# Optimization experiments

Hardware: AMD Instinct MI355X
Metric: run time of the kernel (lower is better)

## Reference

```python
import jax, jax.numpy as jnp
import numpy as np
from jax import lax

ANCHOR_AREAS = (128.0**2, 256.0**2, 512.0**2)
ASPECT_RATIOS = (0.5, 1.0, 2.0)
STRIDE = 32.0                      # resnet backbone: get_orig_stat maps fm -> input via x*32
PRE_NMS_TOP_N = 2000
POST_NMS_TOP_N = 100
NMS_IOU_T = 0.7
SCORE_T = 0.1
MIN_SCALE = 0.01
BBOX_XFORM_CLIP = float(np.log(1000.0 / 16.0))


def make_anchors(H, W):
    # anchors laid out in (H, W, A) order to match the offset permutation below
    sizes = []
    for area in ANCHOR_AREAS:
        for r in ASPECT_RATIOS:          # aspect_ratio = w / h
            sizes.append((np.sqrt(area * r), np.sqrt(area / r)))
    sizes = jnp.asarray(np.asarray(sizes, dtype=np.float32))  # [A, 2] (w, h)
    cy = (jnp.arange(H, dtype=jnp.float32) + 0.5) * STRIDE
    cx = (jnp.arange(W, dtype=jnp.float32) + 0.5) * STRIDE
    cyg, cxg = jnp.meshgrid(cy, cx, indexing='ij')             # [H, W]
    cxg = cxg[:, :, None]
    cyg = cyg[:, :, None]
    w = sizes[:, 0]
    h = sizes[:, 1]
    anchors = jnp.stack([cxg - w / 2, cyg - h / 2, cxg + w / 2, cyg + h / 2], axis=-1)
    return anchors.reshape(-1, 4)                              # [H*W*A, 4] xyxy


def decode_boxes(anchors, offsets):
    # anchors [N,4], offsets [B,N,4] (tx, ty, tw, th) -> boxes [B,N,4] xyxy
    wa = anchors[:, 2] - anchors[:, 0]
    ha = anchors[:, 3] - anchors[:, 1]
    cxa = anchors[:, 0] + 0.5 * wa
    cya = anchors[:, 1] + 0.5 * ha
    tx, ty = offsets[..., 0], offsets[..., 1]
    tw = jnp.minimum(offsets[..., 2], BBOX_XFORM_CLIP)
    th = jnp.minimum(offsets[..., 3], BBOX_XFORM_CLIP)
    px = tx * wa + cxa
    py = ty * ha + cya
    pw = jnp.exp(tw) * wa
    ph = jnp.exp(th) * ha
    return jnp.stack([px - pw / 2, py - ph / 2, px + pw / 2, py + ph / 2], axis=-1)


def box_iou(a, b):
    area_a = (a[:, 2] - a[:, 0]) * (a[:, 3] - a[:, 1])
    area_b = (b[:, 2] - b[:, 0]) * (b[:, 3] - b[:, 1])
    lt = jnp.maximum(a[:, None, :2], b[None, :, :2])
    rb = jnp.minimum(a[:, None, 2:], b[None, :, 2:])
    wh = jnp.clip(rb - lt, 0.0)
    inter = wh[..., 0] * wh[..., 1]
    return inter / (area_a[:, None] + area_b[None, :] - inter + 1e-9)


def nms_single(boxes, scores):
    # boxes [P,4] sorted by descending score; invalid entries carry score -1
    P = boxes.shape[0]
    iou = box_iou(boxes, boxes)
    idx = jnp.arange(P)

    def body(i, keep):
        sup = (iou[i] > NMS_IOU_T) & (idx > i)
        return jnp.where(keep[i], keep & (~sup), keep)

    keep = lax.stop_gradient(lax.fori_loop(0, P, body, scores > 0.0))
    kept_scores = jnp.where(keep, scores, -1.0)
    top_s, top_i = lax.top_k(kept_scores, POST_NMS_TOP_N)
    return boxes[top_i], top_s


def rpn_forward(features, W1, b1, W2, b2, W3, b3):
    B, Cin, H, W = features.shape
    A = W3.shape[0]
    # 3x3 sliding conv + ReLU
    t = lax.conv_general_dilated(
        features, W1, window_strides=(1, 1), padding='SAME',
        dimension_numbers=('NCHW', 'OIHW', 'NCHW'))
    t = jax.nn.relu(t + b1[None, :, None, None])
    # 1x1 sibling heads as channel contractions
    offs = jnp.einsum('bchw,oc->bohw', t, W2) + b2[None, :, None, None]   # [B, A*4, H, W]
    logits = jnp.einsum('bchw,oc->bohw', t, W3) + b3[None, :, None, None]  # [B, A, H, W]
    # reorder to per-anchor layout (H, W, A)
    offs = offs.reshape(B, A, 4, H, W).transpose(0, 3, 4, 1, 2).reshape(B, -1, 4)
    scores = jax.nn.sigmoid(logits.transpose(0, 2, 3, 1).reshape(B, -1))  # [B, N]
    anchors = make_anchors(H, W)
    boxes = decode_boxes(anchors, offs)                                    # [B, N, 4]
    # clip to image boundary (handle_cross_boundary_boxes during testing)
    img_w, img_h = W * STRIDE, H * STRIDE
    boxes = jnp.stack([
        jnp.clip(boxes[..., 0], 0.0, img_w),
        jnp.clip(boxes[..., 1], 0.0, img_h),
        jnp.clip(boxes[..., 2], 0.0, img_w),
        jnp.clip(boxes[..., 3], 0.0, img_h)], axis=-1)
    # score-threshold + min-scale filtering
    bw = boxes[..., 2] - boxes[..., 0]
    bh = boxes[..., 3] - boxes[..., 1]
    valid = (scores >= SCORE_T) & (bw > MIN_SCALE * img_w) & (bh > MIN_SCALE * img_h)
    masked = jnp.where(valid, scores, -1.0)
    # pre-NMS top-k, then per-image NMS + post-NMS top-n
    top_s, top_i = lax.top_k(masked, PRE_NMS_TOP_N)                        # [B, P]
    top_boxes = jnp.take_along_axis(boxes, top_i[..., None], axis=1)       # [B, P, 4]
    out_boxes, out_scores = jax.vmap(nms_single)(top_boxes, top_s)
    return out_boxes, out_scores                                           # [B,100,4], [B,100]


def setup_inputs() -> dict:
    key = jax.random.key(0)
    ks = jax.random.split(key, 4)
    B, Cin, H, W = 8, 1024, 50, 50
    A = 9
    C = 512
    return {
        'features': jax.random.normal(ks[0], (B, Cin, H, W), jnp.float32),
        'W1': jax.random.normal(ks[1], (C, Cin, 3, 3), jnp.float32) * 0.01,
        'b1': jnp.zeros((C,), jnp.float32),
        'W2': jax.random.normal(ks[2], (A * 4, C), jnp.float32) * 0.01,
        'b2': jnp.zeros((A * 4,), jnp.float32),
        'W3': jax.random.normal(ks[3], (A, C), jnp.float32) * 0.01,
        'b3': jnp.zeros((A,), jnp.float32),
    }


def reference(features, W1, b1, W2, b2, W3, b3):
    return rpn_forward(features, W1, b1, W2, b2, W3, b3)
```

## Files before the change

kernel.cpp:

```cpp
#include <hip/hip_runtime.h>
#include <cstdint>

#define NB 8
#define CIN 1024
#define HDIM 50
#define WDIM 50
#define COUT 512
#define NA 9
#define NANCH (HDIM*WDIM*NA)
#define PRE_N 2000
#define POST_N 100

typedef __attribute__((ext_vector_type(8))) short bf16x8;
typedef __attribute__((ext_vector_type(4))) float f32x4;
typedef __attribute__((ext_vector_type(16))) float f32x16;
typedef __attribute__((ext_vector_type(8))) unsigned short ushort8v;

constexpr size_t TPLANE    = 20578304;
constexpr size_t OFF_TPH   = 0;
constexpr size_t OFF_TPL   = 20578304;
constexpr size_t OFF_BOXES = 41156608;
constexpr size_t OFF_KEYS  = 44036608;
constexpr size_t OFF_TBOX  = 45476608;
constexpr size_t OFF_TS    = 45732608;
constexpr size_t OFF_SUP   = 45796608;
constexpr size_t QDIM      = 2976;
constexpr size_t PLSTRIDE  = QDIM * 8;
constexpr size_t PPLANE    = 48758784;
constexpr size_t OFF_PH    = 49892864;
constexpr size_t OFF_PL    = OFF_PH + PPLANE;
constexpr size_t WPLANE    = 9437184;
constexpr size_t OFF_WH    = 147410432;
constexpr size_t OFF_WL    = OFF_WH + WPLANE;

__device__ __forceinline__ void split2bf16(float v, unsigned short &hi, unsigned short &lo) {
    unsigned int u = __float_as_uint(v);
    unsigned int r = u + 0x7FFFu + ((u >> 16) & 1u);
    hi = (unsigned short)(r >> 16);
    float hf = __uint_as_float(((unsigned int)hi) << 16);
    float lf = v - hf;
    unsigned int u2 = __float_as_uint(lf);
    unsigned int r2 = u2 + 0x7FFFu + ((u2 >> 16) & 1u);
    lo = (unsigned short)(r2 >> 16);
}

__device__ __forceinline__ void gl_lds(const unsigned short* g, unsigned short* l) {
    __builtin_amdgcn_global_load_lds(
        (const __attribute__((address_space(1))) unsigned int*)(const void*)g,
        (__attribute__((address_space(3))) unsigned int*)(void*)l,
        16, 0, 0);
}

struct StageOn  { static constexpr bool value = true;  };
struct StageOff { static constexpr bool value = false; };

__global__ __launch_bounds__(256) void prep_all(const float* __restrict__ f,
                                                const float* __restrict__ W1,
                                                unsigned short* __restrict__ Ph,
                                                unsigned short* __restrict__ Pl,
                                                unsigned short* __restrict__ Wh,
                                                unsigned short* __restrict__ Wl) {
    int blk = blockIdx.x;
    if (blk < 5952) {
        int id = blk * 256 + threadIdx.x;
        int q = id % (int)QDIM; int r = id / (int)QDIM;
        int cic = r % 64; int b = r / 64;
        int pp = q - 53;
        int rr = pp / 52, cc = pp - rr * 52;
        int h = rr - 1, w = cc - 1;
        bool inb = (pp >= 0) && (pp < 2704) && (h >= 0) && (h < HDIM) && (w >= 0) && (w < WDIM);
        ushort8v hv0, lv0, hv1, lv1;
#pragma unroll
        for (int j = 0; j < 16; ++j) {
            float v = 0.f;
            if (inb) v = f[(((size_t)b * CIN + cic * 16 + j) * HDIM + h) * WDIM + w];
            unsigned short hi, lo;
            split2bf16(v, hi, lo);
            if (j < 8) { hv0[j] = hi; lv0[j] = lo; }
            else       { hv1[j - 8] = hi; lv1[j - 8] = lo; }
        }
        size_t b0 = ((size_t)((b * 64 + cic) * 2 + 0)) * PLSTRIDE + (size_t)q * 8;
        size_t b1 = ((size_t)((b * 64 + cic) * 2 + 1)) * PLSTRIDE + (size_t)q * 8;
        *(ushort8v*)&Ph[b0] = hv0;
        *(ushort8v*)&Ph[b1] = hv1;
        *(ushort8v*)&Pl[b0] = lv0;
        *(ushort8v*)&Pl[b1] = lv1;
    } else {
        int id = (blk - 5952) * 256 + threadIdx.x;
        int co = id % 64; int r = id / 64;
        int cic = r % 64; int cot = r / 64;
        int cog = cot * 64 + co;
        const float* src = W1 + ((size_t)cog * CIN + cic * 16) * 9;
        float v[144];
#pragma unroll
        for (int i = 0; i < 36; ++i) {
            float4 x = ((const float4*)src)[i];
            v[i * 4 + 0] = x.x; v[i * 4 + 1] = x.y; v[i * 4 + 2] = x.z; v[i * 4 + 3] = x.w;
        }
#pragma unroll
        for (int tap = 0; tap < 9; ++tap) {
            ushort8v hv0, lv0, hv1, lv1;
#pragma unroll
            for (int j = 0; j < 16; ++j) {
                unsigned short hi, lo;
                split2bf16(v[j * 9 + tap], hi, lo);
                if (j < 8) { hv0[j] = hi; lv0[j] = lo; }
                else       { hv1[j - 8] = hi; lv1[j - 8] = lo; }
            }
            size_t base = (((size_t)(cot * 64 + cic) * 9 + tap) * 2) * 512;
            *(ushort8v*)&Wh[base + co * 8]       = hv0;
            *(ushort8v*)&Wh[base + 512 + co * 8] = hv1;
            *(ushort8v*)&Wl[base + co * 8]       = lv0;
            *(ushort8v*)&Wl[base + 512 + co * 8] = lv1;
        }
    }
}


#define MFMA12(A_, B_)                                                               \
    do {                                                                             \
        _Pragma("unroll") for (int s_ = 0; s_ < 3; ++s_)                             \
        _Pragma("unroll") for (int jm_ = 0; jm_ < 2; ++jm_)                          \
        _Pragma("unroll") for (int jn_ = 0; jn_ < 2; ++jn_) {                        \
            const bf16x8 &av_ = (s_ == 2) ? A_[jm_][1] : A_[jm_][0];                 \
            const bf16x8 &bv_ = (s_ == 1) ? B_[jn_][1] : B_[jn_][0];                 \
            acc[jm_][jn_] = __builtin_amdgcn_mfma_f32_32x32x16_bf16(                 \
                av_, bv_, acc[jm_][jn_], 0, 0, 0);                                   \
        }                                                                            \
    } while (0)

#define LOADF(A_, B_, TL_)                                                           \
    do {                                                                             \
        const int dlt_ = (tg - 1) * 52 + ((TL_) - 1);                                \
        _Pragma("unroll") for (int jm_ = 0; jm_ < 2; ++jm_) {                        \
            int ad_ = ((wv * 2 + jm_) * 32 + lm + dlt_ + 53) * 8;                    \
            A_[jm_][0] = *(const bf16x8*)&bA[(0 * 2 + lk) * 3072 + ad_];             \
            A_[jm_][1] = *(const bf16x8*)&bA[(1 * 2 + lk) * 3072 + ad_];             \
        }                                                                            \
        _Pragma("unroll") for (int jn_ = 0; jn_ < 2; ++jn_) {                        \
            int bd_ = (TL_) * 1024 + lk * 512 + (jn_ * 32 + lm) * 8;                 \
            B_[jn_][0] = *(const bf16x8*)&bB[bd_];                                   \
            B_[jn_][1] = *(const bf16x8*)&bB[3072 + bd_];                            \
        }                                                                            \
    } while (0)

__global__ __launch_bounds__(256, 2) void conv_mfma(const unsigned short* __restrict__ FPh,
                                                    const unsigned short* __restrict__ FPl,
                                                    const unsigned short* __restrict__ WPh,
                                                    const unsigned short* __restrict__ WPl,
                                                    const float* __restrict__ b1,
                                                    unsigned short* __restrict__ Tph,
                                                    unsigned short* __restrict__ Tpl) {
    extern __shared__ unsigned short smem[];
    unsigned short* const Abase = smem;
    unsigned short* const Bbase = smem + 24576;

    int blk = blockIdx.x;
    int logical = (blk & 7) * 88 + (blk >> 3);
    int cot = logical & 7;
    int ptile = (logical >> 3) % 11;
    int b = logical / 88;
    int co0 = cot * 64;
    int P0 = 32 + ptile * 256;

    int t = threadIdx.x, wv = t >> 6, ln = t & 63;
    int lm = ln & 31, lk = ln >> 5;

    f32x16 acc[2][2];
#pragma unroll
    for (int jm = 0; jm < 2; ++jm)
#pragma unroll
        for (int jn = 0; jn < 2; ++jn)
#pragma unroll
            for (int rg = 0; rg < 16; ++rg) acc[jm][jn][rg] = 0.f;

    auto stageA = [&](int buf, int cic, int ac) {
        int hl = ac / 12, lkc = (ac / 6) & 1, s = ac % 6;
        const unsigned short* pl = hl ? FPl : FPh;
        const unsigned short* src = pl
            + ((size_t)((b * 64 + cic) * 2 + lkc)) * PLSTRIDE
            + (size_t)P0 * 8 + s * 512 + ln * 8;
        gl_lds(src, &Abase[buf * 12288 + (hl * 2 + lkc) * 3072 + s * 512]);
    };
    auto stageB = [&](int buf, int cic, int tg, int c) {
        int hl = c / 6, j = c % 6;
        const unsigned short* pl = hl ? WPl : WPh;
        const unsigned short* src = pl + (size_t)(cot * 64 + cic) * 9216
            + (size_t)(tg * 6 + j) * 512 + ln * 8;
        gl_lds(src, &Bbase[buf * 6144 + hl * 3072 + j * 512]);
    };

#pragma unroll
    for (int k = 0; k < 9; ++k) {
        int id = wv * 9 + k;
        if (id < 24) stageA(0, 0, id);
        else         stageB(0, 0, 0, id - 24);
    }
    __syncthreads();

    auto do_cic = [&](int cic, auto stage_c) {
        constexpr bool STAGE = decltype(stage_c)::value;
        int abuf = cic & 1;
#pragma unroll
        for (int tg = 0; tg < 3; ++tg) {
            int bbuf = (cic + tg) & 1;
            if (STAGE || tg < 2) {
                int cicb = (tg == 2) ? cic + 1 : cic;
                int tgn  = (tg == 2) ? 0 : tg + 1;
#pragma unroll
                for (int j = 0; j < 3; ++j) stageB(bbuf ^ 1, cicb, tgn, wv * 3 + j);
            }
            if constexpr (STAGE) {
#pragma unroll
                for (int j = 0; j < 2; ++j) stageA(abuf ^ 1, cic + 1, tg * 8 + wv * 2 + j);
            }
            const unsigned short* bA = Abase + abuf * 12288;
            const unsigned short* bB = Bbase + bbuf * 6144;

            bf16x8 aX[2][2], bX[2][2], aY[2][2], bY[2][2];
            LOADF(aX, bX, 0);
            __builtin_amdgcn_s_setprio(1);
            LOADF(aY, bY, 1);
            MFMA12(aX, bX);
            LOADF(aX, bX, 2);
            MFMA12(aY, bY);
            MFMA12(aX, bX);
            __builtin_amdgcn_s_setprio(0);

            if constexpr (STAGE) {
                __builtin_amdgcn_sched_group_barrier(0x070, 5, 0);
                __builtin_amdgcn_sched_group_barrier(0x100, 8, 0);
#pragma unroll
                for (int g = 0; g < 8; ++g) {
                    __builtin_amdgcn_sched_group_barrier(0x008, 3, 0);
                    __builtin_amdgcn_sched_group_barrier(0x100, 2, 0);
                }
                __builtin_amdgcn_sched_group_barrier(0x008, 12, 0);
            }
            __syncthreads();
        }
    };

#pragma unroll 1
    for (int cic = 0; cic < 63; ++cic) do_cic(cic, StageOn{});
    do_cic(63, StageOff{});

#pragma unroll
    for (int jn = 0; jn < 2; ++jn) {
        int co = co0 + jn * 32 + lm;
        float bv = b1[co];
#pragma unroll
        for (int jm = 0; jm < 2; ++jm) {
#pragma unroll
            for (int rg = 0; rg < 16; ++rg) {
                int mrow = (rg & 3) + 8 * (rg >> 2) + 4 * lk;
                int pp = P0 + (wv * 2 + jm) * 32 + mrow;
                int rr = pp / 52, cc = pp - rr * 52;
                int h = rr - 1, w = cc - 1;
                if ((unsigned)h < HDIM && (unsigned)w < WDIM) {
                    float v = fmaxf(acc[jm][jn][rg] + bv, 0.f);
                    unsigned short hi, lo;
                    split2bf16(v, hi, lo);
                    int px = b * 2500 + h * 50 + w;
                    size_t sa = (((((size_t)(px >> 7) * 16 + (co >> 5)) * 8 + ((px >> 4) & 7)) * 4
                                  + ((co >> 3) & 3)) * 16 + (px & 15)) * 8 + (co & 7);
                    Tph[sa] = hi;
                    Tpl[sa] = lo;
                }
            }
        }
    }
}

__global__ __launch_bounds__(256) void proj_decode_mfma(const unsigned short* __restrict__ Tph,
                                                        const unsigned short* __restrict__ Tpl,
                                                        const float* __restrict__ W2,
                                                        const float* __restrict__ b2,
                                                        const float* __restrict__ W3,
                                                        const float* __restrict__ b3,
                                                        float* __restrict__ boxes,
                                                        unsigned long long* __restrict__ keys) {
    __shared__ unsigned short sTh[4096], sTl[4096];
    __shared__ unsigned short sWh[1536], sWl[1536];
    __shared__ float pout[128 * 46];

    int blk = blockIdx.x;
    int px0 = blk * 128;
    int t = threadIdx.x, wv = t >> 6, ln = t & 63;
    int lm = ln & 15, q = ln >> 4;

    f32x4 acc[2][3];
#pragma unroll
    for (int jm = 0; jm < 2; ++jm)
#pragma unroll
        for (int nf = 0; nf < 3; ++nf) acc[jm][nf] = (f32x4){0.f, 0.f, 0.f, 0.f};

#pragma unroll 1
    for (int cc16 = 0; cc16 < 16; ++cc16) {
        __syncthreads();
        size_t base = ((size_t)blk * 16 + cc16) * 4096;
        if (wv == 0) {
#pragma unroll
            for (int s = 0; s < 4; ++s) gl_lds(Tph + base + s * 512 + ln * 8, &sTh[s * 512]);
        } else if (wv == 1) {
#pragma unroll
            for (int s = 4; s < 8; ++s) gl_lds(Tph + base + s * 512 + ln * 8, &sTh[s * 512]);
        } else if (wv == 2) {
#pragma unroll
            for (int s = 0; s < 4; ++s) gl_lds(Tpl + base + s * 512 + ln * 8, &sTl[s * 512]);
        } else {
#pragma unroll
            for (int s = 4; s < 8; ++s) gl_lds(Tpl + base + s * 512 + ln * 8, &sTl[s * 512]);
        }
        int c0 = cc16 * 32;
        for (int idx = t; idx < 1536; idx += 256) {
            int o = idx >> 5, ci = idx & 31;
            float v = 0.f;
            if (o < 36) v = W2[o * 512 + c0 + ci];
            else if (o < 45) v = W3[(o - 36) * 512 + c0 + ci];
            unsigned short hi, lo;
            split2bf16(v, hi, lo);
            int ad = (((o >> 4) * 4 + (ci >> 3)) * 16 + (o & 15)) * 8 + (ci & 7);
            sWh[ad] = hi; sWl[ad] = lo;
        }
        __syncthreads();

        bf16x8 a[2][2], bb[3][2];
#pragma unroll
        for (int jm = 0; jm < 2; ++jm) {
            int mf = wv * 2 + jm;
            int ad = ((mf * 4 + q) * 16 + lm) * 8;
            a[jm][0] = *(const bf16x8*)&sTh[ad];
            a[jm][1] = *(const bf16x8*)&sTl[ad];
        }
#pragma unroll
        for (int nf = 0; nf < 3; ++nf) {
            int ad = ((nf * 4 + q) * 16 + lm) * 8;
            bb[nf][0] = *(const bf16x8*)&sWh[ad];
            bb[nf][1] = *(const bf16x8*)&sWl[ad];
        }
#pragma unroll
        for (int jm = 0; jm < 2; ++jm)
#pragma unroll
            for (int nf = 0; nf < 3; ++nf) {
                acc[jm][nf] = __builtin_amdgcn_mfma_f32_16x16x32_bf16(a[jm][0], bb[nf][0], acc[jm][nf], 0, 0, 0);
                acc[jm][nf] = __builtin_amdgcn_mfma_f32_16x16x32_bf16(a[jm][0], bb[nf][1], acc[jm][nf], 0, 0, 0);
                acc[jm][nf] = __builtin_amdgcn_mfma_f32_16x16x32_bf16(a[jm][1], bb[nf][0], acc[jm][nf], 0, 0, 0);
            }
    }
    __syncthreads();
#pragma unroll
    for (int jm = 0; jm < 2; ++jm)
#pragma unroll
        for (int nf = 0; nf < 3; ++nf) {
            int o = nf * 16 + lm;
            if (o < 45) {
                float bias = (o < 36) ? b2[o] : b3[o - 36];
#pragma unroll
                for (int rg = 0; rg < 4; ++rg) {
                    int pxl = (wv * 2 + jm) * 16 + q * 4 + rg;
                    pout[pxl * 46 + o] = acc[jm][nf][rg] + bias;
                }
            }
        }
    __syncthreads();

    const float AW[9] = {90.50966799187809f, 128.0f, 181.01933598375618f,
                         181.01933598375618f, 256.0f, 362.03867196751236f,
                         362.03867196751236f, 512.0f, 724.0773439350247f};
    const float AH[9] = {181.01933598375618f, 128.0f, 90.50966799187809f,
                         362.03867196751236f, 256.0f, 181.01933598375618f,
                         724.0773439350247f, 512.0f, 362.03867196751236f};
    const float CLIPV = 4.135166556742356f;
    const float IMG = 1600.0f;

    for (int it = t; it < 128 * 9; it += 256) {
        int pxl = it / 9, a = it - pxl * 9;
        int pxg = px0 + pxl;
        if (pxg >= 20000) continue;
        int b = pxg / 2500, rem = pxg % 2500;
        int h = rem / 50, w = rem % 50;

        float tx = pout[pxl * 46 + a * 4 + 0];
        float ty = pout[pxl * 46 + a * 4 + 1];
        float tw = pout[pxl * 46 + a * 4 + 2];
        float th = pout[pxl * 46 + a * 4 + 3];
        float lg = pout[pxl * 46 + 36 + a];

        float s = 1.0f / (1.0f + expf(-lg));

        float cx = ((float)w + 0.5f) * 32.0f;
        float cy = ((float)h + 0.5f) * 32.0f;
        float x1a = cx - 0.5f * AW[a];
        float x2a = cx + 0.5f * AW[a];
        float y1a = cy - 0.5f * AH[a];
        float y2a = cy + 0.5f * AH[a];
        float waf = x2a - x1a;
        float haf = y2a - y1a;
        float cxa = x1a + 0.5f * waf;
        float cya = y1a + 0.5f * haf;

        float twc = tw < CLIPV ? tw : CLIPV;
        float thc = th < CLIPV ? th : CLIPV;
        float pxc = tx * waf + cxa;
        float pyc = ty * haf + cya;
        float pw  = expf(twc) * waf;
        float ph  = expf(thc) * haf;

        float x1 = pxc - 0.5f * pw;
        float y1 = pyc - 0.5f * ph;
        float x2 = pxc + 0.5f * pw;
        float y2 = pyc + 0.5f * ph;
        x1 = fminf(fmaxf(x1, 0.f), IMG);
        y1 = fminf(fmaxf(y1, 0.f), IMG);
        x2 = fminf(fmaxf(x2, 0.f), IMG);
        y2 = fminf(fmaxf(y2, 0.f), IMG);

        float bw = x2 - x1, bh = y2 - y1;
        bool valid = (s >= 0.1f) && (bw > 16.0f) && (bh > 16.0f);
        float m = valid ? s : -1.0f;

        int idx = (h * WDIM + w) * NA + a;
        size_t gi = (size_t)b * NANCH + idx;
        ((float4*)boxes)[gi] = make_float4(x1, y1, x2, y2);
        unsigned int u = __float_as_uint(m);
        unsigned int k32 = (u & 0x80000000u) ? ~u : (u | 0x80000000u);
        keys[gi] = ((unsigned long long)k32 << 15) | (unsigned long long)(32767 - idx);
    }
}

__global__ __launch_bounds__(1024) void select_sort_kernel(const unsigned long long* __restrict__ keys,
                                                           const float* __restrict__ boxes,
                                                           float* __restrict__ top_boxes,
                                                           float* __restrict__ top_s) {
    int b = blockIdx.x;
    int t = threadIdx.x;
    int wv = t >> 6;
    const unsigned long long* kb = keys + (size_t)b * NANCH;

    __shared__ unsigned int whist[16][256];
    __shared__ unsigned int hist[256];
    __shared__ int s_chosen, s_rnew, s_done;
    __shared__ unsigned int s_cnt;
    __shared__ unsigned long long skeys[2048];

    const int widths[6] = {8, 8, 8, 8, 8, 7};
    unsigned long long prefix = 0;
    int bitsdone = 0;
    int r = PRE_N;

    if (t == 0) s_done = 0;

    for (int p = 0; p < 6; ++p) {
        int width = widths[p];
        int bins = 1 << width;
        int shift = 47 - bitsdone - width;
        for (int i = t; i < 16 * 256; i += 1024) ((unsigned int*)whist)[i] = 0;
        __syncthreads();
        for (int i = t; i < NANCH; i += 1024) {
            unsigned long long k = kb[i];
            if ((k >> (47 - bitsdone)) == prefix)
                atomicAdd(&whist[wv][(unsigned)((k >> shift) & (unsigned long long)(bins - 1))], 1u);
        }
        __syncthreads();
        if (t < bins) {
            unsigned int s = 0;
#pragma unroll
            for (int w = 0; w < 16; ++w) s += whist[w][t];
            hist[t] = s;
        }
        __syncthreads();
        if (t == 0) {
            int acc = 0, chosen = 0, rnew = 1;
            for (int d = bins - 1; d >= 0; --d) {
                int hv = (int)hist[d];
                if (acc + hv >= r) {
                    chosen = d; rnew = r - acc;
                    if ((PRE_N - r) + acc + hv <= 2048) s_done = 1;
                    break;
                }
                acc += hv;
            }
            s_chosen = chosen;
            s_rnew = rnew;
        }
        __syncthreads();
        prefix = (prefix << width) | (unsigned long long)s_chosen;
        bitsdone += width;
        r = s_rnew;
        __syncthreads();
        if (s_done) break;
    }
    unsigned long long Kst = prefix << (47 - bitsdone);

    if (t == 0) s_cnt = 0;
    __syncthreads();
    for (int i = t; i < NANCH; i += 1024) {
        unsigned long long k = kb[i];
        if (k >= Kst) {
            unsigned int p = atomicAdd(&s_cnt, 1u);
            if (p < 2048) skeys[p] = k;
        }
    }
    __syncthreads();
    unsigned int cnt = s_cnt;
    for (int i = t; i < 2048; i += 1024)
        if (i >= (int)cnt) skeys[i] = 0ull;
    for (int k = 2; k <= 2048; k <<= 1) {
        for (int j = k >> 1; j > 0; j >>= 1) {
            __syncthreads();
            for (int i = t; i < 2048; i += 1024) {
                int l = i ^ j;
                if (l > i) {
                    unsigned long long a = skeys[i], c = skeys[l];
                    bool up = ((i & k) == 0);
                    if (up ? (a < c) : (a > c)) { skeys[i] = c; skeys[l] = a; }
                }
            }
        }
    }
    __syncthreads();
    for (int i = t; i < PRE_N; i += 1024) {
        unsigned long long k = skeys[i];
        unsigned int k32 = (unsigned int)(k >> 15);
        float m = (k32 & 0x80000000u) ? __uint_as_float(k32 & 0x7FFFFFFFu)
                                      : __uint_as_float(~k32);
        unsigned int idx = 32767u - (unsigned int)(k & 32767ull);
        size_t gi = (size_t)b * NANCH + idx;
        top_s[b * PRE_N + i] = m;
        ((float4*)top_boxes)[b * PRE_N + i] = ((const float4*)boxes)[gi];
    }
}

__global__ __launch_bounds__(256) void sup_kernel(const float* __restrict__ top_boxes,
                                                  unsigned long long* __restrict__ supm) {
    int blk = blockIdx.x;
    int b = blk / 125;
    int chunk = blk % 125;
    int t = threadIdx.x;

    __shared__ float bx1[PRE_N], by1[PRE_N], bx2[PRE_N], by2[PRE_N];
    for (int i = t; i < PRE_N; i += 256) {
        float4 v = ((const float4*)top_boxes)[b * PRE_N + i];
        bx1[i] = v.x; by1[i] = v.y; bx2[i] = v.z; by2[i] = v.w;
    }
    __syncthreads();

    int wave = t >> 6, lane = t & 63;
    for (int rr = 0; rr < 4; ++rr) {
        int i = chunk * 16 + wave * 4 + rr;
        float ax1 = bx1[i], ay1 = by1[i], ax2 = bx2[i], ay2 = by2[i];
        float aarea = (ax2 - ax1) * (ay2 - ay1);
        for (int jw = 0; jw < 32; ++jw) {
            int j = jw * 64 + lane;
            bool sup = false;
            if (j > i && j < PRE_N) {
                float jx1 = bx1[j], jy1 = by1[j], jx2 = bx2[j], jy2 = by2[j];
                float ix1 = fmaxf(ax1, jx1), iy1 = fmaxf(ay1, jy1);
                float ix2 = fminf(ax2, jx2), iy2 = fminf(ay2, jy2);
                float iw = fmaxf(ix2 - ix1, 0.f);
                float ih = fmaxf(iy2 - iy1, 0.f);
                float inter = iw * ih;
                float barea = (jx2 - jx1) * (jy2 - jy1);
                float iou = inter / (aarea + barea - inter + 1e-9f);
                sup = iou > 0.7f;
            }
            unsigned long long m = __ballot(sup);
            if (lane == 0) supm[((size_t)b * PRE_N + i) * 32 + jw] = m;
        }
    }
}

__global__ __launch_bounds__(256) void nms_fin_kernel(const float* __restrict__ top_s,
                                                      const unsigned long long* __restrict__ supm,
                                                      const float* __restrict__ top_boxes,
                                                      float* __restrict__ out) {
    int b = blockIdx.x;
    int t = threadIdx.x;
    __shared__ unsigned int kw[64];
    __shared__ int wpre[65];

    if (t < 64) {
        int lane = t;
        unsigned int alive = 0;
        for (int q = 0; q < 32; ++q) {
            int i = lane * 32 + q;
            if (i < PRE_N && top_s[b * PRE_N + i] > 0.f) alive |= (1u << q);
        }
        const unsigned long long* sm = supm + (size_t)b * PRE_N * 32;
        const unsigned int* sup32 = (const unsigned int*)sm;

        for (int tt = 0; tt < 32; ++tt) {
            unsigned int alo = __shfl(alive, 2 * tt);
            unsigned int ahi = __shfl(alive, 2 * tt + 1);
            unsigned long long talive = (unsigned long long)alo | ((unsigned long long)ahi << 32);
            int i_row = tt * 64 + lane;
            unsigned long long rm = (i_row < PRE_N) ? sm[(size_t)i_row * 32 + tt] : 0ull;

            unsigned long long kept = 0, rem = talive;
            while (rem) {
                int j = __builtin_ctzll(rem);
                kept |= (1ull << j);
                unsigned long long rmj = __shfl(rm, j);
                rem &= ~rmj;
                rem &= ~(1ull << j);
            }

            unsigned int oracc = 0;
            unsigned long long kk = kept;
            while (kk) {
                int j0 = __builtin_ctzll(kk); kk &= kk - 1;
                int j1 = -1, j2 = -1, j3 = -1, j4 = -1, j5 = -1, j6 = -1, j7 = -1;
                if (kk) { j1 = __builtin_ctzll(kk); kk &= kk - 1; }
                if (kk) { j2 = __builtin_ctzll(kk); kk &= kk - 1; }
                if (kk) { j3 = __builtin_ctzll(kk); kk &= kk - 1; }
                if (kk) { j4 = __builtin_ctzll(kk); kk &= kk - 1; }
                if (kk) { j5 = __builtin_ctzll(kk); kk &= kk - 1; }
                if (kk) { j6 = __builtin_ctzll(kk); kk &= kk - 1; }
                if (kk) { j7 = __builtin_ctzll(kk); kk &= kk - 1; }
                unsigned int v0 = sup32[(size_t)(tt * 64 + j0) * 64 + lane];
                unsigned int v1 = (j1 >= 0) ? sup32[(size_t)(tt * 64 + j1) * 64 + lane] : 0u;
                unsigned int v2 = (j2 >= 0) ? sup32[(size_t)(tt * 64 + j2) * 64 + lane] : 0u;
                unsigned int v3 = (j3 >= 0) ? sup32[(size_t)(tt * 64 + j3) * 64 + lane] : 0u;
                unsigned int v4 = (j4 >= 0) ? sup32[(size_t)(tt * 64 + j4) * 64 + lane] : 0u;
                unsigned int v5 = (j5 >= 0) ? sup32[(size_t)(tt * 64 + j5) * 64 + lane] : 0u;
                unsigned int v6 = (j6 >= 0) ? sup32[(size_t)(tt * 64 + j6) * 64 + lane] : 0u;
                unsigned int v7 = (j7 >= 0) ? sup32[(size_t)(tt * 64 + j7) * 64 + lane] : 0u;
                oracc |= (v0 | v1) | (v2 | v3) | (v4 | v5) | (v6 | v7);
            }
            alive &= ~oracc;
            if (lane == 2 * tt)     alive = (unsigned int)kept;
            if (lane == 2 * tt + 1) alive = (unsigned int)(kept >> 32);
        }
        kw[lane] = alive;
    }
    __syncthreads();
    if (t == 0) {
        int run = 0;
        for (int w = 0; w < 64; ++w) { wpre[w] = run; run += __popc(kw[w]); }
        wpre[64] = run;
    }
    __syncthreads();
    int total = wpre[64];
    float* out_boxes  = out;
    float* out_scores = out + NB * POST_N * 4;
    for (int i = t; i < PRE_N; i += 256) {
        unsigned int w = kw[i >> 5];
        bool kept = (w >> (i & 31)) & 1u;
        int rk = wpre[i >> 5] + __popc(w & ((1u << (i & 31)) - 1u));
        int pos = kept ? rk : total + (i - rk);
        if (pos < POST_N) {
            out_scores[b * POST_N + pos] = kept ? top_s[b * PRE_N + i] : -1.0f;
            ((float4*)out_boxes)[b * POST_N + pos] = ((const float4*)top_boxes)[b * PRE_N + i];
        }
    }
}

extern "C" void kernel_launch(void* const* d_in, const int* in_sizes, int n_in,
                              void* d_out, int out_size, void* d_ws, size_t ws_size,
                              hipStream_t stream) {
    const float* features = (const float*)d_in[0];
    const float* W1 = (const float*)d_in[1];
    const float* b1 = (const float*)d_in[2];
    const float* W2 = (const float*)d_in[3];
    const float* b2 = (const float*)d_in[4];
    const float* W3 = (const float*)d_in[5];
    const float* b3 = (const float*)d_in[6];
    float* out = (float*)d_out;
    char* ws = (char*)d_ws;

    unsigned short* Tph = (unsigned short*)(ws + OFF_TPH);
    unsigned short* Tpl = (unsigned short*)(ws + OFF_TPL);
    float* boxes   = (float*)(ws + OFF_BOXES);
    unsigned long long* keys = (unsigned long long*)(ws + OFF_KEYS);
    float* top_boxes = (float*)(ws + OFF_TBOX);
    float* top_s     = (float*)(ws + OFF_TS);
    unsigned long long* supm = (unsigned long long*)(ws + OFF_SUP);
    unsigned short* FPh = (unsigned short*)(ws + OFF_PH);
    unsigned short* FPl = (unsigned short*)(ws + OFF_PL);
    unsigned short* WPh = (unsigned short*)(ws + OFF_WH);
    unsigned short* WPl = (unsigned short*)(ws + OFF_WL);

    static bool conv_attr_set = false;
    if (!conv_attr_set) {
        hipFuncSetAttribute(reinterpret_cast<const void*>(&conv_mfma),
                            hipFuncAttributeMaxDynamicSharedMemorySize, 73728);
        conv_attr_set = true;
    }

    prep_all<<<6080, 256, 0, stream>>>(features, W1, FPh, FPl, WPh, WPl);
    conv_mfma<<<704, 256, 73728, stream>>>(FPh, FPl, WPh, WPl, b1, Tph, Tpl);
    proj_decode_mfma<<<157, 256, 0, stream>>>(Tph, Tpl, W2, b2, W3, b3, boxes, keys);
    select_sort_kernel<<<NB, 1024, 0, stream>>>(keys, boxes, top_boxes, top_s);
    sup_kernel<<<NB * 125, 256, 0, stream>>>(top_boxes, supm);
    nms_fin_kernel<<<NB, 256, 0, stream>>>(top_s, supm, top_boxes, out);
}
```

Before: 1.001 ms.

## Prefetch conv A fragments across tap groups and fuse first radix histogram into decode

The conv main loop now loads A-operand register fragments for all three taps of the next tap group (or next channel chunk) during the current group's MFMAs. It double-buffers these register sets (aX/aY) and redistributes the A staging across the three phases. The decode kernel also builds the first-pass top-byte histogram of the sort keys with global atomics, so the select kernel skips one full scan of the keys. This costs more registers at 2-blocks occupancy, adds a memset, and reuses the FPh workspace region for the histogram (it is dead after conv).

Result: slower. 1.135 ms (+13.4%).

```diff
diff --git a/kernel.cpp b/kernel.cpp
--- a/kernel.cpp
+++ b/kernel.cpp
@@ -32,6 +32,7 @@
 constexpr size_t WPLANE    = 9437184;
 constexpr size_t OFF_WH    = 147410432;
 constexpr size_t OFF_WL    = OFF_WH + WPLANE;
+constexpr size_t OFF_GH    = OFF_PH;
 
 __device__ __forceinline__ void split2bf16(float v, unsigned short &hi, unsigned short &lo) {
     unsigned int u = __float_as_uint(v);
@@ -50,9 +51,6 @@
         (__attribute__((address_space(3))) unsigned int*)(void*)l,
         16, 0, 0);
 }
-
-struct StageOn  { static constexpr bool value = true;  };
-struct StageOff { static constexpr bool value = false; };
 
 __global__ __launch_bounds__(256) void prep_all(const float* __restrict__ f,
                                                 const float* __restrict__ W1,
@@ -117,31 +115,90 @@
 }
 
 
-#define MFMA12(A_, B_)                                                               \
+#define LOADA(SET_, SRC_, TG_)                                                       \
+    do {                                                                             \
+        _Pragma("unroll") for (int tl_ = 0; tl_ < 3; ++tl_) {                        \
+            const int dlt_ = ((TG_) - 1) * 52 + (tl_ - 1);                           \
+            _Pragma("unroll") for (int jm_ = 0; jm_ < 2; ++jm_) {                    \
+                int ad_ = ((wv * 2 + jm_) * 32 + lm + dlt_ + 53) * 8;                \
+                SET_[tl_][jm_][0] = *(const bf16x8*)&(SRC_)[lk * 3072 + ad_];        \
+                SET_[tl_][jm_][1] = *(const bf16x8*)&(SRC_)[(2 + lk) * 3072 + ad_];  \
+            }                                                                        \
+        }                                                                            \
+    } while (0)
+
+#define LOADB(B_, BB_, TL_)                                                          \
+    do {                                                                             \
+        _Pragma("unroll") for (int jn_ = 0; jn_ < 2; ++jn_) {                        \
+            int bd_ = (TL_) * 1024 + lk * 512 + (jn_ * 32 + lm) * 8;                 \
+            B_[jn_][0] = *(const bf16x8*)&(BB_)[bd_];                                \
+            B_[jn_][1] = *(const bf16x8*)&(BB_)[3072 + bd_];                         \
+        }                                                                            \
+    } while (0)
+
+#define MFMA12A(SET_, TL_, B_)                                                       \
     do {                                                                             \
         _Pragma("unroll") for (int s_ = 0; s_ < 3; ++s_)                             \
         _Pragma("unroll") for (int jm_ = 0; jm_ < 2; ++jm_)                          \
         _Pragma("unroll") for (int jn_ = 0; jn_ < 2; ++jn_) {                        \
-            const bf16x8 &av_ = (s_ == 2) ? A_[jm_][1] : A_[jm_][0];                 \
+            const bf16x8 &av_ = (s_ == 2) ? SET_[TL_][jm_][1] : SET_[TL_][jm_][0];   \
             const bf16x8 &bv_ = (s_ == 1) ? B_[jn_][1] : B_[jn_][0];                 \
             acc[jm_][jn_] = __builtin_amdgcn_mfma_f32_32x32x16_bf16(                 \
                 av_, bv_, acc[jm_][jn_], 0, 0, 0);                                   \
         }                                                                            \
     } while (0)
 
-#define LOADF(A_, B_, TL_)                                                           \
+#define PHASE(CUR_, NXT_, CIC_, TG_, PRESRC_, NTG_, STAGEON_)                        \
     do {                                                                             \
-        const int dlt_ = (tg - 1) * 52 + ((TL_) - 1);                                \
-        _Pragma("unroll") for (int jm_ = 0; jm_ < 2; ++jm_) {                        \
-            int ad_ = ((wv * 2 + jm_) * 32 + lm + dlt_ + 53) * 8;                    \
-            A_[jm_][0] = *(const bf16x8*)&bA[(0 * 2 + lk) * 3072 + ad_];             \
-            A_[jm_][1] = *(const bf16x8*)&bA[(1 * 2 + lk) * 3072 + ad_];             \
+        const int bbuf_ = ((CIC_) + (TG_)) & 1;                                      \
+        const unsigned short* bB_ = Bbase + bbuf_ * 6144;                            \
+        if ((STAGEON_) || (TG_) < 2) {                                               \
+            int cicb_ = ((TG_) == 2) ? (CIC_) + 1 : (CIC_);                          \
+            int tgn_  = ((TG_) == 2) ? 0 : (TG_) + 1;                                \
+            _Pragma("unroll") for (int j_ = 0; j_ < 3; ++j_)                         \
+                stageB(bbuf_ ^ 1, cicb_, tgn_, wv * 3 + j_);                         \
         }                                                                            \
-        _Pragma("unroll") for (int jn_ = 0; jn_ < 2; ++jn_) {                        \
-            int bd_ = (TL_) * 1024 + lk * 512 + (jn_ * 32 + lm) * 8;                 \
-            B_[jn_][0] = *(const bf16x8*)&bB[bd_];                                   \
-            B_[jn_][1] = *(const bf16x8*)&bB[3072 + bd_];                            \
+        if (STAGEON_) {                                                              \
+            if ((TG_) == 0) {                                                        \
+                _Pragma("unroll") for (int j_ = 0; j_ < 3; ++j_)                     \
+                    stageA((((CIC_) & 1) ^ 1), (CIC_) + 1, wv * 3 + j_);             \
+            } else if ((TG_) == 1) {                                                 \
+                _Pragma("unroll") for (int j_ = 0; j_ < 2; ++j_)                     \
+                    stageA((((CIC_) & 1) ^ 1), (CIC_) + 1, 12 + wv * 2 + j_);        \
+            } else {                                                                 \
+                stageA((((CIC_) & 1) ^ 1), (CIC_) + 1, 20 + wv);                     \
+            }                                                                        \
         }                                                                            \
+        bf16x8 b0_[2][2], b1_[2][2];                                                 \
+        LOADB(b0_, bB_, 0);                                                          \
+        __builtin_amdgcn_s_setprio(1);                                               \
+        LOADB(b1_, bB_, 1);                                                          \
+        MFMA12A(CUR_, 0, b0_);                                                       \
+        LOADB(b0_, bB_, 2);                                                          \
+        if ((STAGEON_) || (TG_) < 2) LOADA(NXT_, PRESRC_, NTG_);                     \
+        MFMA12A(CUR_, 1, b1_);                                                       \
+        MFMA12A(CUR_, 2, b0_);                                                       \
+        __builtin_amdgcn_s_setprio(0);                                               \
+        if (STAGEON_) {                                                              \
+            const int nv_ = ((TG_) == 0) ? 6 : ((TG_) == 1) ? 5 : 4;                 \
+            __builtin_amdgcn_sched_group_barrier(0x070, nv_, 0);                     \
+            __builtin_amdgcn_sched_group_barrier(0x100, 8, 0);                       \
+            _Pragma("unroll") for (int g_ = 0; g_ < 8; ++g_) {                       \
+                __builtin_amdgcn_sched_group_barrier(0x008, 3, 0);                   \
+                __builtin_amdgcn_sched_group_barrier(0x100, 2, 0);                   \
+            }                                                                        \
+            __builtin_amdgcn_sched_group_barrier(0x008, 12, 0);                      \
+        }                                                                            \
+        __syncthreads();                                                             \
+    } while (0)
+
+#define DO_CIC(CUR_, NXT_, CIC_, STAGEON_)                                           \
+    do {                                                                             \
+        const unsigned short* bAc_ = Abase + ((CIC_) & 1) * 12288;                   \
+        const unsigned short* bAn_ = Abase + (((CIC_) & 1) ^ 1) * 12288;             \
+        PHASE(CUR_, NXT_, CIC_, 0, bAc_, 1, STAGEON_);                               \
+        PHASE(NXT_, CUR_, CIC_, 1, bAc_, 2, STAGEON_);                               \
+        PHASE(CUR_, NXT_, CIC_, 2, bAn_, 0, STAGEON_);                               \
     } while (0)
 
 __global__ __launch_bounds__(256, 2) void conv_mfma(const unsigned short* __restrict__ FPh,
@@ -174,13 +231,15 @@
 #pragma unroll
             for (int rg = 0; rg < 16; ++rg) acc[jm][jn][rg] = 0.f;
 
-    auto stageA = [&](int buf, int cic, int ac) {
-        int hl = ac / 12, lkc = (ac / 6) & 1, s = ac % 6;
+    auto stageA = [&](int buf, int cic, int ci) {
+        int r = (ci < 20) ? (ci & 3) : (ci - 20);
+        int s = (ci < 20) ? (ci >> 2) : 5;
+        int hl = r >> 1, lkc = r & 1;
         const unsigned short* pl = hl ? FPl : FPh;
         const unsigned short* src = pl
             + ((size_t)((b * 64 + cic) * 2 + lkc)) * PLSTRIDE
             + (size_t)P0 * 8 + s * 512 + ln * 8;
-        gl_lds(src, &Abase[buf * 12288 + (hl * 2 + lkc) * 3072 + s * 512]);
+        gl_lds(src, &Abase[buf * 12288 + r * 3072 + s * 512]);
     };
     auto stageB = [&](int buf, int cic, int tg, int c) {
         int hl = c / 6, j = c % 6;
@@ -198,52 +257,16 @@
     }
     __syncthreads();
 
-    auto do_cic = [&](int cic, auto stage_c) {
-        constexpr bool STAGE = decltype(stage_c)::value;
-        int abuf = cic & 1;
-#pragma unroll
-        for (int tg = 0; tg < 3; ++tg) {
-            int bbuf = (cic + tg) & 1;
-            if (STAGE || tg < 2) {
-                int cicb = (tg == 2) ? cic + 1 : cic;
-                int tgn  = (tg == 2) ? 0 : tg + 1;
-#pragma unroll
-                for (int j = 0; j < 3; ++j) stageB(bbuf ^ 1, cicb, tgn, wv * 3 + j);
-            }
-            if constexpr (STAGE) {
-#pragma unroll
-                for (int j = 0; j < 2; ++j) stageA(abuf ^ 1, cic + 1, tg * 8 + wv * 2 + j);
-            }
-            const unsigned short* bA = Abase + abuf * 12288;
-            const unsigned short* bB = Bbase + bbuf * 6144;
-
-            bf16x8 aX[2][2], bX[2][2], aY[2][2], bY[2][2];
-            LOADF(aX, bX, 0);
-            __builtin_amdgcn_s_setprio(1);
-            LOADF(aY, bY, 1);
-            MFMA12(aX, bX);
-            LOADF(aX, bX, 2);
-            MFMA12(aY, bY);
-            MFMA12(aX, bX);
-            __builtin_amdgcn_s_setprio(0);
-
-            if constexpr (STAGE) {
-                __builtin_amdgcn_sched_group_barrier(0x070, 5, 0);
-                __builtin_amdgcn_sched_group_barrier(0x100, 8, 0);
-#pragma unroll
-                for (int g = 0; g < 8; ++g) {
-                    __builtin_amdgcn_sched_group_barrier(0x008, 3, 0);
-                    __builtin_amdgcn_sched_group_barrier(0x100, 2, 0);
-                }
-                __builtin_amdgcn_sched_group_barrier(0x008, 12, 0);
-            }
-            __syncthreads();
-        }
-    };
+    bf16x8 aX[3][2][2], aY[3][2][2];
+    LOADA(aX, Abase, 0);
 
 #pragma unroll 1
-    for (int cic = 0; cic < 63; ++cic) do_cic(cic, StageOn{});
-    do_cic(63, StageOff{});
+    for (int cc = 0; cc < 31; ++cc) {
+        DO_CIC(aX, aY, 2 * cc,     1);
+        DO_CIC(aY, aX, 2 * cc + 1, 1);
+    }
+    DO_CIC(aX, aY, 62, 1);
+    DO_CIC(aY, aX, 63, 0);
 
 #pragma unroll
     for (int jn = 0; jn < 2; ++jn) {
@@ -279,7 +302,8 @@
                                                         const float* __restrict__ W3,
                                                         const float* __restrict__ b3,
                                                         float* __restrict__ boxes,
-                                                        unsigned long long* __restrict__ keys) {
+                                                        unsigned long long* __restrict__ keys,
+                                                        unsigned int* __restrict__ ghist) {
     __shared__ unsigned short sTh[4096], sTl[4096];
     __shared__ unsigned short sWh[1536], sWl[1536];
     __shared__ float pout[128 * 46];
@@ -425,14 +449,17 @@
         ((float4*)boxes)[gi] = make_float4(x1, y1, x2, y2);
         unsigned int u = __float_as_uint(m);
         unsigned int k32 = (u & 0x80000000u) ? ~u : (u | 0x80000000u);
-        keys[gi] = ((unsigned long long)k32 << 15) | (unsigned long long)(32767 - idx);
+        unsigned long long kv = ((unsigned long long)k32 << 15) | (unsigned long long)(32767 - idx);
+        keys[gi] = kv;
+        atomicAdd(&ghist[b * 256 + (unsigned)((kv >> 39) & 255ull)], 1u);
     }
 }
 
 __global__ __launch_bounds__(1024) void select_sort_kernel(const unsigned long long* __restrict__ keys,
                                                            const float* __restrict__ boxes,
                                                            float* __restrict__ top_boxes,
-                                                           float* __restrict__ top_s) {
+                                                           float* __restrict__ top_s,
+                                                           const unsigned int* __restrict__ ghist) {
     int b = blockIdx.x;
     int t = threadIdx.x;
     int wv = t >> 6;
@@ -455,21 +482,26 @@
         int width = widths[p];
         int bins = 1 << width;
         int shift = 47 - bitsdone - width;
-        for (int i = t; i < 16 * 256; i += 1024) ((unsigned int*)whist)[i] = 0;
-        __syncthreads();
-        for (int i = t; i < NANCH; i += 1024) {
-            unsigned long long k = kb[i];
-            if ((k >> (47 - bitsdone)) == prefix)
-                atomicAdd(&whist[wv][(unsigned)((k >> shift) & (unsigned long long)(bins - 1))], 1u);
-        }
-        __syncthreads();
-        if (t < bins) {
-            unsigned int s = 0;
-#pragma unroll
-            for (int w = 0; w < 16; ++w) s += whist[w][t];
-            hist[t] = s;
-        }
-        __syncthreads();
+        if (p == 0) {
+            if (t < 256) hist[t] = ghist[b * 256 + t];
+            __syncthreads();
+        } else {
+            for (int i = t; i < 16 * 256; i += 1024) ((unsigned int*)whist)[i] = 0;
+            __syncthreads();
+            for (int i = t; i < NANCH; i += 1024) {
+                unsigned long long k = kb[i];
+                if ((k >> (47 - bitsdone)) == prefix)
+                    atomicAdd(&whist[wv][(unsigned)((k >> shift) & (unsigned long long)(bins - 1))], 1u);
+            }
+            __syncthreads();
+            if (t < bins) {
+                unsigned int s = 0;
+#pragma unroll
+                for (int w = 0; w < 16; ++w) s += whist[w][t];
+                hist[t] = s;
+            }
+            __syncthreads();
+        }
         if (t == 0) {
             int acc = 0, chosen = 0, rnew = 1;
             for (int d = bins - 1; d >= 0; --d) {
@@ -680,6 +712,7 @@
     unsigned short* FPl = (unsigned short*)(ws + OFF_PL);
     unsigned short* WPh = (unsigned short*)(ws + OFF_WH);
     unsigned short* WPl = (unsigned short*)(ws + OFF_WL);
+    unsigned int* ghist = (unsigned int*)(ws + OFF_GH);
 
     static bool conv_attr_set = false;
     if (!conv_attr_set) {
@@ -690,8 +723,9 @@
 
     prep_all<<<6080, 256, 0, stream>>>(features, W1, FPh, FPl, WPh, WPl);
     conv_mfma<<<704, 256, 73728, stream>>>(FPh, FPl, WPh, WPl, b1, Tph, Tpl);
-    proj_decode_mfma<<<157, 256, 0, stream>>>(Tph, Tpl, W2, b2, W3, b3, boxes, keys);
-    select_sort_kernel<<<NB, 1024, 0, stream>>>(keys, boxes, top_boxes, top_s);
+    hipMemsetAsync(ghist, 0, NB * 256 * sizeof(unsigned int), stream);
+    proj_decode_mfma<<<157, 256, 0, stream>>>(Tph, Tpl, W2, b2, W3, b3, boxes, keys, ghist);
+    select_sort_kernel<<<NB, 1024, 0, stream>>>(keys, boxes, top_boxes, top_s, ghist);
     sup_kernel<<<NB * 125, 256, 0, stream>>>(top_boxes, supm);
     nms_fin_kernel<<<NB, 256, 0, stream>>>(top_s, supm, top_boxes, out);
 }
```
